# Kernel tuning notes

Measured on AMD Instinct MI355X. Metric: run time of the kernel, lower is better.

The kernel has to match this reference:

```python
import jax, jax.numpy as jnp
import numpy as np

N_NODES = 50000
N_EDGES = 800000
VOCAB = 1000
EMBED = 64
HIDDEN = 64
N_CLASSES = 10
N_GRAPHS = 512


def setup_inputs() -> dict:
    key = jax.random.key(0)
    ks = jax.random.split(key, 10)
    tokens = jax.random.randint(ks[0], (N_NODES,), 0, VOCAB)
    edge_index = jax.random.randint(ks[1], (2, N_EDGES), 0, N_NODES)
    batch = jnp.sort(jax.random.randint(ks[2], (N_NODES,), 0, N_GRAPHS))
    emb = jax.random.normal(ks[3], (VOCAB, EMBED), jnp.float32) * 0.02
    emb = emb.at[0].set(0.0)  # padding_idx=0
    W1 = jax.random.normal(ks[4], (EMBED, HIDDEN), jnp.float32) * (1.0 / np.sqrt(EMBED))
    b1 = jnp.zeros((HIDDEN,), jnp.float32)
    W2 = jax.random.normal(ks[5], (HIDDEN, HIDDEN), jnp.float32) * (1.0 / np.sqrt(HIDDEN))
    b2 = jnp.zeros((HIDDEN,), jnp.float32)
    lin_W = jax.random.normal(ks[6], (HIDDEN, N_CLASSES), jnp.float32) * (1.0 / np.sqrt(HIDDEN))
    lin_b = jnp.zeros((N_CLASSES,), jnp.float32)
    return {"tokens": tokens, "edge_index": edge_index, "batch": batch,
            "emb": emb, "W1": W1, "b1": b1, "W2": W2, "b2": b2,
            "lin_W": lin_W, "lin_b": lin_b}


def _gcn_conv(x, src, dst, W, b, n_nodes):
    # PyG GCNConv: add self-loops, symmetric normalization D^-1/2 (A+I) D^-1/2
    ones = jnp.ones((src.shape[0],), x.dtype)
    deg = jax.ops.segment_sum(ones, dst, num_segments=n_nodes) + 1.0  # self-loop
    dis = jnp.where(deg > 0, jax.lax.rsqrt(deg), 0.0)
    h = x @ W  # linear first (no bias)
    coef = dis[src] * dis[dst]                      # [E]
    msg = h[src] * coef[:, None]                    # gather + scale
    agg = jax.ops.segment_sum(msg, dst, num_segments=n_nodes)
    agg = agg + h * (dis * dis)[:, None]            # self-loop message
    return agg + b


def reference(tokens, edge_index, batch, emb, W1, b1, W2, b2, lin_W, lin_b):
    src, dst = edge_index[0], edge_index[1]
    x = emb[tokens]                                  # [N, EMBED]
    x = jax.nn.relu(_gcn_conv(x, src, dst, W1, b1, N_NODES))
    x = jax.nn.relu(_gcn_conv(x, src, dst, W2, b2, N_NODES))
    # global_mean_pool over batch ids
    sums = jax.ops.segment_sum(x, batch, num_segments=N_GRAPHS)
    cnts = jax.ops.segment_sum(jnp.ones((x.shape[0],), x.dtype), batch, num_segments=N_GRAPHS)
    pooled = sums / jnp.maximum(cnts, 1.0)[:, None]  # [G, HIDDEN]
    return pooled @ lin_W + lin_b
```

## Files before the change

### kernel.cpp

```cpp
#include <hip/hip_runtime.h>

#define NGRAPHS 512
#define D 64
#define NCLS 10
#define MAXDEG 64
#define MDSH 6

__global__ void k_deg(const int* __restrict__ dst, int* __restrict__ degi,
                      int* __restrict__ rank, int E) {
  int i = blockIdx.x * blockDim.x + threadIdx.x;
  if (i < E) rank[i] = atomicAdd(&degi[dst[i]], 1);
}

__global__ __launch_bounds__(256) void k_fused2(
    const int* __restrict__ src, const int* __restrict__ dst,
    const int* __restrict__ rank, const int* __restrict__ tokens,
    int2* __restrict__ ec2, int E,
    const int* __restrict__ degi, float* __restrict__ dis, int n,
    const float* __restrict__ emb, const float* __restrict__ W1,
    float4* __restrict__ ht4, float4* __restrict__ h2pad, int ntok,
    int fillBlocks, int disBlocks, int tokBlocks) {
  if (blockIdx.x < fillBlocks) {
    int e = blockIdx.x * 256 + threadIdx.x;
    if (e < E) {
      int s = src[e];
      int rk = rank[e];
      if (rk < MAXDEG)
        ec2[((size_t)dst[e] << MDSH) + rk] = make_int2(s, tokens[s]);
    }
    return;
  }
  if (blockIdx.x < fillBlocks + disBlocks) {
    int i = (blockIdx.x - fillBlocks) * 256 + threadIdx.x;
    if (i < n) dis[i] = rsqrtf((float)degi[i] + 1.0f);
    if (blockIdx.x == fillBlocks) {
      int t = threadIdx.x;
      if (t == 0) dis[n] = 0.0f;
      float4 z = make_float4(0.f, 0.f, 0.f, 0.f);
      if (t < 16) h2pad[((size_t)n << 4) + t] = z;
      else if (t < 32) ht4[((size_t)ntok << 4) + (t - 16)] = z;
    }
    return;
  }
  __shared__ float Ws[64 * 64];
  int tid = threadIdx.x;
  for (int i = tid; i < 64 * 64; i += 256) Ws[i] = W1[i];
  __syncthreads();
  const float4* Ws4 = (const float4*)Ws;
  int w = tid >> 6, lane = tid & 63;
  int cg = lane & 15;
  int kb = lane & 48;
  int bid = blockIdx.x - fillBlocks - disBlocks;
  for (int tok = bid * 4 + w; tok < ntok; tok += tokBlocks * 4) {
    float xval = emb[(size_t)tok * D + lane];
    float4 acc = make_float4(0.f, 0.f, 0.f, 0.f);
#pragma unroll
    for (int p = 0; p < 16; ++p) {
      float xv = __shfl(xval, kb + p, 64);
      float4 wv = Ws4[(kb + p) * 16 + cg];
      acc.x += xv * wv.x; acc.y += xv * wv.y;
      acc.z += xv * wv.z; acc.w += xv * wv.w;
    }
    acc.x += __shfl_xor(acc.x, 16, 64); acc.y += __shfl_xor(acc.y, 16, 64);
    acc.z += __shfl_xor(acc.z, 16, 64); acc.w += __shfl_xor(acc.w, 16, 64);
    acc.x += __shfl_xor(acc.x, 32, 64); acc.y += __shfl_xor(acc.y, 32, 64);
    acc.z += __shfl_xor(acc.z, 32, 64); acc.w += __shfl_xor(acc.w, 32, 64);
    if (lane < 16) ht4[(size_t)tok * 16 + cg] = acc;
  }
}

__global__ __launch_bounds__(256) void k_agg1g(const float4* __restrict__ ht4,
                                               const int2* __restrict__ ec2,
                                               const int* __restrict__ degi,
                                               const int* __restrict__ tokens,
                                               const float* __restrict__ dis,
                                               const float4* __restrict__ b14,
                                               const float* __restrict__ W2,
                                               float4* __restrict__ h2, int n,
                                               int ntok) {
  __shared__ float Ws[64 * 64];
  int tid = threadIdx.x;
  for (int i = tid; i < 64 * 64; i += 256) Ws[i] = W2[i];
  __syncthreads();
  const float4* Ws4 = (const float4*)Ws;
  int w = tid >> 6, lane = tid & 63;
  int slot = lane >> 4, cg = lane & 15;
  int kb = lane & 48;
  for (int node = blockIdx.x * 4 + w; node < n; node += gridDim.x * 4) {
    int deg = min(degi[node], MAXDEG);
    int beg = node << MDSH;
    int endp = beg + deg;
    float4 acc = make_float4(0.f, 0.f, 0.f, 0.f);
    int rounds = (deg + 31) >> 5;
    int j = beg + slot;
    for (int r = 0; r < rounds; ++r, j += 32) {
      int i0 = j, i1 = j + 4, i2 = j + 8, i3 = j + 12,
          i4 = j + 16, i5 = j + 20, i6 = j + 24, i7 = j + 28;
      int2 e0 = ec2[i0], e1 = ec2[i1], e2 = ec2[i2], e3 = ec2[i3];
      int2 e4 = ec2[i4], e5 = ec2[i5], e6 = ec2[i6], e7 = ec2[i7];
      int s0 = i0 < endp ? e0.x : n, t0 = i0 < endp ? e0.y : ntok;
      int s1 = i1 < endp ? e1.x : n, t1 = i1 < endp ? e1.y : ntok;
      int s2 = i2 < endp ? e2.x : n, t2 = i2 < endp ? e2.y : ntok;
      int s3 = i3 < endp ? e3.x : n, t3 = i3 < endp ? e3.y : ntok;
      int s4 = i4 < endp ? e4.x : n, t4 = i4 < endp ? e4.y : ntok;
      int s5 = i5 < endp ? e5.x : n, t5 = i5 < endp ? e5.y : ntok;
      int s6 = i6 < endp ? e6.x : n, t6 = i6 < endp ? e6.y : ntok;
      int s7 = i7 < endp ? e7.x : n, t7 = i7 < endp ? e7.y : ntok;
      float w0 = dis[s0], w1 = dis[s1], w2 = dis[s2], w3 = dis[s3];
      float w4 = dis[s4], w5 = dis[s5], w6 = dis[s6], w7 = dis[s7];
      float4 v0 = ht4[((size_t)t0 << 4) + cg];
      float4 v1 = ht4[((size_t)t1 << 4) + cg];
      float4 v2 = ht4[((size_t)t2 << 4) + cg];
      float4 v3 = ht4[((size_t)t3 << 4) + cg];
      float4 v4 = ht4[((size_t)t4 << 4) + cg];
      float4 v5 = ht4[((size_t)t5 << 4) + cg];
      float4 v6 = ht4[((size_t)t6 << 4) + cg];
      float4 v7 = ht4[((size_t)t7 << 4) + cg];
      acc.x += w0 * v0.x + w1 * v1.x + w2 * v2.x + w3 * v3.x
             + w4 * v4.x + w5 * v5.x + w6 * v6.x + w7 * v7.x;
      acc.y += w0 * v0.y + w1 * v1.y + w2 * v2.y + w3 * v3.y
             + w4 * v4.y + w5 * v5.y + w6 * v6.y + w7 * v7.y;
      acc.z += w0 * v0.z + w1 * v1.z + w2 * v2.z + w3 * v3.z
             + w4 * v4.z + w5 * v5.z + w6 * v6.z + w7 * v7.z;
      acc.w += w0 * v0.w + w1 * v1.w + w2 * v2.w + w3 * v3.w
             + w4 * v4.w + w5 * v5.w + w6 * v6.w + w7 * v7.w;
    }
    acc.x += __shfl_xor(acc.x, 16, 64); acc.y += __shfl_xor(acc.y, 16, 64);
    acc.z += __shfl_xor(acc.z, 16, 64); acc.w += __shfl_xor(acc.w, 16, 64);
    acc.x += __shfl_xor(acc.x, 32, 64); acc.y += __shfl_xor(acc.y, 32, 64);
    acc.z += __shfl_xor(acc.z, 32, 64); acc.w += __shfl_xor(acc.w, 32, 64);
    float dd = dis[node];
    float4 vd = ht4[((size_t)tokens[node] << 4) + cg];
    float4 bv = b14[cg];
    float4 x2;
    x2.x = dd * fmaxf(dd * (acc.x + dd * vd.x) + bv.x, 0.f);
    x2.y = dd * fmaxf(dd * (acc.y + dd * vd.y) + bv.y, 0.f);
    x2.z = dd * fmaxf(dd * (acc.z + dd * vd.z) + bv.z, 0.f);
    x2.w = dd * fmaxf(dd * (acc.w + dd * vd.w) + bv.w, 0.f);
    float4 g = make_float4(0.f, 0.f, 0.f, 0.f);
#pragma unroll
    for (int p = 0; p < 4; ++p) {
      int sl = (kb >> 2) + p;
      float xv0 = __shfl(x2.x, sl, 64);
      float xv1 = __shfl(x2.y, sl, 64);
      float xv2 = __shfl(x2.z, sl, 64);
      float xv3 = __shfl(x2.w, sl, 64);
      float4 w0 = Ws4[(kb + 4 * p + 0) * 16 + cg];
      float4 w1 = Ws4[(kb + 4 * p + 1) * 16 + cg];
      float4 w2 = Ws4[(kb + 4 * p + 2) * 16 + cg];
      float4 w3 = Ws4[(kb + 4 * p + 3) * 16 + cg];
      g.x += xv0 * w0.x + xv1 * w1.x + xv2 * w2.x + xv3 * w3.x;
      g.y += xv0 * w0.y + xv1 * w1.y + xv2 * w2.y + xv3 * w3.y;
      g.z += xv0 * w0.z + xv1 * w1.z + xv2 * w2.z + xv3 * w3.z;
      g.w += xv0 * w0.w + xv1 * w1.w + xv2 * w2.w + xv3 * w3.w;
    }
    g.x += __shfl_xor(g.x, 16, 64); g.y += __shfl_xor(g.y, 16, 64);
    g.z += __shfl_xor(g.z, 16, 64); g.w += __shfl_xor(g.w, 16, 64);
    g.x += __shfl_xor(g.x, 32, 64); g.y += __shfl_xor(g.y, 32, 64);
    g.z += __shfl_xor(g.z, 32, 64); g.w += __shfl_xor(g.w, 32, 64);
    if (lane < 16) h2[((size_t)node << 4) + cg] = g;
  }
}

__global__ __launch_bounds__(256) void k_aggs(const float4* __restrict__ h4,
                                              const int2* __restrict__ ec2,
                                              const int* __restrict__ degi,
                                              const float* __restrict__ dis,
                                              const float4* __restrict__ b24,
                                              float4* __restrict__ out, int n) {
  int tid = blockIdx.x * blockDim.x + threadIdx.x;
  int node = tid >> 6;
  int lane = tid & 63;
  int slot = lane >> 4;
  int cg = lane & 15;
  if (node >= n) return;
  int deg = min(degi[node], MAXDEG);
  int beg = node << MDSH;
  int endp = beg + deg;
  float4 acc = make_float4(0.f, 0.f, 0.f, 0.f);
  int rounds = (deg + 31) >> 5;
  int j = beg + slot;
  for (int r = 0; r < rounds; ++r, j += 32) {
    int i0 = j, i1 = j + 4, i2 = j + 8, i3 = j + 12,
        i4 = j + 16, i5 = j + 20, i6 = j + 24, i7 = j + 28;
    int2 e0 = ec2[i0], e1 = ec2[i1], e2 = ec2[i2], e3 = ec2[i3];
    int2 e4 = ec2[i4], e5 = ec2[i5], e6 = ec2[i6], e7 = ec2[i7];
    int s0 = i0 < endp ? e0.x : n;
    int s1 = i1 < endp ? e1.x : n;
    int s2 = i2 < endp ? e2.x : n;
    int s3 = i3 < endp ? e3.x : n;
    int s4 = i4 < endp ? e4.x : n;
    int s5 = i5 < endp ? e5.x : n;
    int s6 = i6 < endp ? e6.x : n;
    int s7 = i7 < endp ? e7.x : n;
    float4 v0 = h4[((size_t)s0 << 4) + cg];
    float4 v1 = h4[((size_t)s1 << 4) + cg];
    float4 v2 = h4[((size_t)s2 << 4) + cg];
    float4 v3 = h4[((size_t)s3 << 4) + cg];
    float4 v4 = h4[((size_t)s4 << 4) + cg];
    float4 v5 = h4[((size_t)s5 << 4) + cg];
    float4 v6 = h4[((size_t)s6 << 4) + cg];
    float4 v7 = h4[((size_t)s7 << 4) + cg];
    acc.x += ((v0.x + v1.x) + (v2.x + v3.x)) + ((v4.x + v5.x) + (v6.x + v7.x));
    acc.y += ((v0.y + v1.y) + (v2.y + v3.y)) + ((v4.y + v5.y) + (v6.y + v7.y));
    acc.z += ((v0.z + v1.z) + (v2.z + v3.z)) + ((v4.z + v5.z) + (v6.z + v7.z));
    acc.w += ((v0.w + v1.w) + (v2.w + v3.w)) + ((v4.w + v5.w) + (v6.w + v7.w));
  }
  acc.x += __shfl_xor(acc.x, 16, 64); acc.y += __shfl_xor(acc.y, 16, 64);
  acc.z += __shfl_xor(acc.z, 16, 64); acc.w += __shfl_xor(acc.w, 16, 64);
  acc.x += __shfl_xor(acc.x, 32, 64); acc.y += __shfl_xor(acc.y, 32, 64);
  acc.z += __shfl_xor(acc.z, 32, 64); acc.w += __shfl_xor(acc.w, 32, 64);
  if (slot == 0) {
    float dd = dis[node];
    float4 hv = h4[((size_t)node << 4) + cg];
    float4 bv = b24[cg];
    acc.x = fmaxf(dd * (acc.x + hv.x) + bv.x, 0.f);
    acc.y = fmaxf(dd * (acc.y + hv.y) + bv.y, 0.f);
    acc.z = fmaxf(dd * (acc.z + hv.z) + bv.z, 0.f);
    acc.w = fmaxf(dd * (acc.w + hv.w) + bv.w, 0.f);
    out[((size_t)node << 4) + cg] = acc;
  }
}

__device__ __forceinline__ int lower_bound(const int* __restrict__ a, int n, int v) {
  int lo = 0, hi = n;
  while (lo < hi) {
    int m = (lo + hi) >> 1;
    if (a[m] < v) lo = m + 1; else hi = m;
  }
  return lo;
}

__global__ __launch_bounds__(256) void k_poolfinal(const float* __restrict__ x,
                                                   const int* __restrict__ batch,
                                                   const float* __restrict__ lw,
                                                   const float* __restrict__ lb,
                                                   float* __restrict__ out, int n) {
  __shared__ float red[4][64];
  __shared__ float pooled[64];
  int g = blockIdx.x;
  int s = lower_bound(batch, n, g);
  int e = lower_bound(batch, n, g + 1);
  int w = threadIdx.x >> 6, lane = threadIdx.x & 63;
  float acc = 0.f;
  for (int i = s + w; i < e; i += 4) acc += x[(size_t)i * D + lane];
  red[w][lane] = acc;
  __syncthreads();
  if (w == 0) {
    float v = red[0][lane] + red[1][lane] + red[2][lane] + red[3][lane];
    pooled[lane] = v / fmaxf((float)(e - s), 1.0f);
  }
  __syncthreads();
  if (threadIdx.x < NCLS) {
    int c = threadIdx.x;
    float a = lb[c];
#pragma unroll
    for (int k = 0; k < D; ++k) a += pooled[k] * lw[k * NCLS + c];
    out[g * NCLS + c] = a;
  }
}

extern "C" void kernel_launch(void* const* d_in, const int* in_sizes, int n_in,
                              void* d_out, int out_size, void* d_ws, size_t ws_size,
                              hipStream_t stream) {
  const int* tokens = (const int*)d_in[0];
  const int* edge   = (const int*)d_in[1];
  const int* batch  = (const int*)d_in[2];
  const float* emb  = (const float*)d_in[3];
  const float* W1   = (const float*)d_in[4];
  const float* b1   = (const float*)d_in[5];
  const float* W2   = (const float*)d_in[6];
  const float* b2   = (const float*)d_in[7];
  const float* lw   = (const float*)d_in[8];
  const float* lb   = (const float*)d_in[9];
  float* out = (float*)d_out;

  const int N = in_sizes[0];
  const int E = in_sizes[1] / 2;
  const int ntok = in_sizes[3] / D;
  const int* src  = edge;
  const int* dstv = edge + E;

  char* ws = (char*)d_ws;
  size_t off = 0;
  auto alloc = [&](size_t bytes) {
    void* p = ws + off;
    off += (bytes + 255) & ~(size_t)255;
    return p;
  };
  float* A    = (float*)alloc((size_t)(N + 1) * D * sizeof(float));
  float* B    = (float*)alloc((size_t)N * D * sizeof(float));
  int2*  ec2  = (int2*)alloc((size_t)N * MAXDEG * sizeof(int2));
  int*   rank = (int*)alloc((size_t)E * sizeof(int));
  float* dis  = (float*)alloc((size_t)(N + 1) * sizeof(float));
  int*   degi = (int*)alloc((size_t)N * sizeof(int));
  float* ht   = (float*)alloc((size_t)(ntok + 1) * D * sizeof(float));

  hipMemsetAsync(degi, 0, (size_t)N * sizeof(int), stream);

  k_deg<<<(E + 255) / 256, 256, 0, stream>>>(dstv, degi, rank, E);

  const int fillBlocks = (E + 255) / 256;
  const int disBlocks = (N + 255) / 256;
  const int tokBlocks = (ntok + 3) / 4;
  k_fused2<<<fillBlocks + disBlocks + tokBlocks, 256, 0, stream>>>(
      src, dstv, rank, tokens, ec2, E, degi, dis, N, emb, W1, (float4*)ht,
      (float4*)A, ntok, fillBlocks, disBlocks, tokBlocks);

  k_agg1g<<<2048, 256, 0, stream>>>((const float4*)ht, ec2, degi, tokens, dis,
                                    (const float4*)b1, W2, (float4*)A, N, ntok);

  const int nodeBlocks = (N + 3) / 4;
  k_aggs<<<nodeBlocks, 256, 0, stream>>>((const float4*)A, ec2, degi, dis,
                                         (const float4*)b2, (float4*)B, N);

  k_poolfinal<<<NGRAPHS, 256, 0, stream>>>(B, batch, lw, lb, out, N);
}
```

Measured before the change: 157.6 us.

## Split layer-1 aggregation and W2 GEMM into separate kernels

The fused kernel that aggregated layer-1 messages and then applied W2 per node is split in two. One kernel does the one-node-per-wave aggregation with bias, ReLU and scaling and writes the result to a buffer. A second persistent kernel then multiplies that buffer by W2 held in shared memory. This lets the aggregation run as a flat, non-persistent grid without the shared-memory load, at the cost of an extra launch and an extra N×64 write and read round-trip through memory.

Result: slower. 161.3 us (+2.4%).

```diff
diff --git a/kernel.cpp b/kernel.cpp
--- a/kernel.cpp
+++ b/kernel.cpp
@@ -69,96 +69,101 @@
   }
 }
 
-__global__ __launch_bounds__(256) void k_agg1g(const float4* __restrict__ ht4,
+__global__ __launch_bounds__(256) void k_agg1t(const float4* __restrict__ ht4,
                                                const int2* __restrict__ ec2,
                                                const int* __restrict__ degi,
                                                const int* __restrict__ tokens,
                                                const float* __restrict__ dis,
                                                const float4* __restrict__ b14,
-                                               const float* __restrict__ W2,
-                                               float4* __restrict__ h2, int n,
+                                               float4* __restrict__ out, int n,
                                                int ntok) {
+  int tid = blockIdx.x * blockDim.x + threadIdx.x;
+  int node = tid >> 6;
+  int lane = tid & 63;
+  int slot = lane >> 4;
+  int cg = lane & 15;
+  if (node >= n) return;
+  int deg = min(degi[node], MAXDEG);
+  int beg = node << MDSH;
+  int endp = beg + deg;
+  float4 acc = make_float4(0.f, 0.f, 0.f, 0.f);
+  int rounds = (deg + 31) >> 5;
+  int j = beg + slot;
+  for (int r = 0; r < rounds; ++r, j += 32) {
+    int i0 = j, i1 = j + 4, i2 = j + 8, i3 = j + 12,
+        i4 = j + 16, i5 = j + 20, i6 = j + 24, i7 = j + 28;
+    int2 e0 = ec2[i0], e1 = ec2[i1], e2 = ec2[i2], e3 = ec2[i3];
+    int2 e4 = ec2[i4], e5 = ec2[i5], e6 = ec2[i6], e7 = ec2[i7];
+    int s0 = i0 < endp ? e0.x : n, t0 = i0 < endp ? e0.y : ntok;
+    int s1 = i1 < endp ? e1.x : n, t1 = i1 < endp ? e1.y : ntok;
+    int s2 = i2 < endp ? e2.x : n, t2 = i2 < endp ? e2.y : ntok;
+    int s3 = i3 < endp ? e3.x : n, t3 = i3 < endp ? e3.y : ntok;
+    int s4 = i4 < endp ? e4.x : n, t4 = i4 < endp ? e4.y : ntok;
+    int s5 = i5 < endp ? e5.x : n, t5 = i5 < endp ? e5.y : ntok;
+    int s6 = i6 < endp ? e6.x : n, t6 = i6 < endp ? e6.y : ntok;
+    int s7 = i7 < endp ? e7.x : n, t7 = i7 < endp ? e7.y : ntok;
+    float w0 = dis[s0], w1 = dis[s1], w2 = dis[s2], w3 = dis[s3];
+    float w4 = dis[s4], w5 = dis[s5], w6 = dis[s6], w7 = dis[s7];
+    float4 v0 = ht4[((size_t)t0 << 4) + cg];
+    float4 v1 = ht4[((size_t)t1 << 4) + cg];
+    float4 v2 = ht4[((size_t)t2 << 4) + cg];
+    float4 v3 = ht4[((size_t)t3 << 4) + cg];
+    float4 v4 = ht4[((size_t)t4 << 4) + cg];
+    float4 v5 = ht4[((size_t)t5 << 4) + cg];
+    float4 v6 = ht4[((size_t)t6 << 4) + cg];
+    float4 v7 = ht4[((size_t)t7 << 4) + cg];
+    acc.x += w0 * v0.x + w1 * v1.x + w2 * v2.x + w3 * v3.x
+           + w4 * v4.x + w5 * v5.x + w6 * v6.x + w7 * v7.x;
+    acc.y += w0 * v0.y + w1 * v1.y + w2 * v2.y + w3 * v3.y
+           + w4 * v4.y + w5 * v5.y + w6 * v6.y + w7 * v7.y;
+    acc.z += w0 * v0.z + w1 * v1.z + w2 * v2.z + w3 * v3.z
+           + w4 * v4.z + w5 * v5.z + w6 * v6.z + w7 * v7.z;
+    acc.w += w0 * v0.w + w1 * v1.w + w2 * v2.w + w3 * v3.w
+           + w4 * v4.w + w5 * v5.w + w6 * v6.w + w7 * v7.w;
+  }
+  acc.x += __shfl_xor(acc.x, 16, 64); acc.y += __shfl_xor(acc.y, 16, 64);
+  acc.z += __shfl_xor(acc.z, 16, 64); acc.w += __shfl_xor(acc.w, 16, 64);
+  acc.x += __shfl_xor(acc.x, 32, 64); acc.y += __shfl_xor(acc.y, 32, 64);
+  acc.z += __shfl_xor(acc.z, 32, 64); acc.w += __shfl_xor(acc.w, 32, 64);
+  if (slot == 0) {
+    float dd = dis[node];
+    float4 vd = ht4[((size_t)tokens[node] << 4) + cg];
+    float4 bv = b14[cg];
+    float4 r;
+    r.x = dd * fmaxf(dd * (acc.x + dd * vd.x) + bv.x, 0.f);
+    r.y = dd * fmaxf(dd * (acc.y + dd * vd.y) + bv.y, 0.f);
+    r.z = dd * fmaxf(dd * (acc.z + dd * vd.z) + bv.z, 0.f);
+    r.w = dd * fmaxf(dd * (acc.w + dd * vd.w) + bv.w, 0.f);
+    out[((size_t)node << 4) + cg] = r;
+  }
+}
+
+__global__ __launch_bounds__(256) void k_gemmp(const float* __restrict__ x,
+                                               const float* __restrict__ W,
+                                               float4* __restrict__ o4, int n) {
   __shared__ float Ws[64 * 64];
   int tid = threadIdx.x;
-  for (int i = tid; i < 64 * 64; i += 256) Ws[i] = W2[i];
+  for (int i = tid; i < 64 * 64; i += 256) Ws[i] = W[i];
   __syncthreads();
   const float4* Ws4 = (const float4*)Ws;
   int w = tid >> 6, lane = tid & 63;
-  int slot = lane >> 4, cg = lane & 15;
+  int cg = lane & 15;
   int kb = lane & 48;
   for (int node = blockIdx.x * 4 + w; node < n; node += gridDim.x * 4) {
-    int deg = min(degi[node], MAXDEG);
-    int beg = node << MDSH;
-    int endp = beg + deg;
+    float xval = x[(size_t)node * D + lane];
     float4 acc = make_float4(0.f, 0.f, 0.f, 0.f);
-    int rounds = (deg + 31) >> 5;
-    int j = beg + slot;
-    for (int r = 0; r < rounds; ++r, j += 32) {
-      int i0 = j, i1 = j + 4, i2 = j + 8, i3 = j + 12,
-          i4 = j + 16, i5 = j + 20, i6 = j + 24, i7 = j + 28;
-      int2 e0 = ec2[i0], e1 = ec2[i1], e2 = ec2[i2], e3 = ec2[i3];
-      int2 e4 = ec2[i4], e5 = ec2[i5], e6 = ec2[i6], e7 = ec2[i7];
-      int s0 = i0 < endp ? e0.x : n, t0 = i0 < endp ? e0.y : ntok;
-      int s1 = i1 < endp ? e1.x : n, t1 = i1 < endp ? e1.y : ntok;
-      int s2 = i2 < endp ? e2.x : n, t2 = i2 < endp ? e2.y : ntok;
-      int s3 = i3 < endp ? e3.x : n, t3 = i3 < endp ? e3.y : ntok;
-      int s4 = i4 < endp ? e4.x : n, t4 = i4 < endp ? e4.y : ntok;
-      int s5 = i5 < endp ? e5.x : n, t5 = i5 < endp ? e5.y : ntok;
-      int s6 = i6 < endp ? e6.x : n, t6 = i6 < endp ? e6.y : ntok;
-      int s7 = i7 < endp ? e7.x : n, t7 = i7 < endp ? e7.y : ntok;
-      float w0 = dis[s0], w1 = dis[s1], w2 = dis[s2], w3 = dis[s3];
-      float w4 = dis[s4], w5 = dis[s5], w6 = dis[s6], w7 = dis[s7];
-      float4 v0 = ht4[((size_t)t0 << 4) + cg];
-      float4 v1 = ht4[((size_t)t1 << 4) + cg];
-      float4 v2 = ht4[((size_t)t2 << 4) + cg];
-      float4 v3 = ht4[((size_t)t3 << 4) + cg];
-      float4 v4 = ht4[((size_t)t4 << 4) + cg];
-      float4 v5 = ht4[((size_t)t5 << 4) + cg];
-      float4 v6 = ht4[((size_t)t6 << 4) + cg];
-      float4 v7 = ht4[((size_t)t7 << 4) + cg];
-      acc.x += w0 * v0.x + w1 * v1.x + w2 * v2.x + w3 * v3.x
-             + w4 * v4.x + w5 * v5.x + w6 * v6.x + w7 * v7.x;
-      acc.y += w0 * v0.y + w1 * v1.y + w2 * v2.y + w3 * v3.y
-             + w4 * v4.y + w5 * v5.y + w6 * v6.y + w7 * v7.y;
-      acc.z += w0 * v0.z + w1 * v1.z + w2 * v2.z + w3 * v3.z
-             + w4 * v4.z + w5 * v5.z + w6 * v6.z + w7 * v7.z;
-      acc.w += w0 * v0.w + w1 * v1.w + w2 * v2.w + w3 * v3.w
-             + w4 * v4.w + w5 * v5.w + w6 * v6.w + w7 * v7.w;
+#pragma unroll
+    for (int p = 0; p < 16; ++p) {
+      float xv = __shfl(xval, kb + p, 64);
+      float4 wv = Ws4[(kb + p) * 16 + cg];
+      acc.x += xv * wv.x; acc.y += xv * wv.y;
+      acc.z += xv * wv.z; acc.w += xv * wv.w;
     }
     acc.x += __shfl_xor(acc.x, 16, 64); acc.y += __shfl_xor(acc.y, 16, 64);
     acc.z += __shfl_xor(acc.z, 16, 64); acc.w += __shfl_xor(acc.w, 16, 64);
     acc.x += __shfl_xor(acc.x, 32, 64); acc.y += __shfl_xor(acc.y, 32, 64);
     acc.z += __shfl_xor(acc.z, 32, 64); acc.w += __shfl_xor(acc.w, 32, 64);
-    float dd = dis[node];
-    float4 vd = ht4[((size_t)tokens[node] << 4) + cg];
-    float4 bv = b14[cg];
-    float4 x2;
-    x2.x = dd * fmaxf(dd * (acc.x + dd * vd.x) + bv.x, 0.f);
-    x2.y = dd * fmaxf(dd * (acc.y + dd * vd.y) + bv.y, 0.f);
-    x2.z = dd * fmaxf(dd * (acc.z + dd * vd.z) + bv.z, 0.f);
-    x2.w = dd * fmaxf(dd * (acc.w + dd * vd.w) + bv.w, 0.f);
-    float4 g = make_float4(0.f, 0.f, 0.f, 0.f);
-#pragma unroll
-    for (int p = 0; p < 4; ++p) {
-      int sl = (kb >> 2) + p;
-      float xv0 = __shfl(x2.x, sl, 64);
-      float xv1 = __shfl(x2.y, sl, 64);
-      float xv2 = __shfl(x2.z, sl, 64);
-      float xv3 = __shfl(x2.w, sl, 64);
-      float4 w0 = Ws4[(kb + 4 * p + 0) * 16 + cg];
-      float4 w1 = Ws4[(kb + 4 * p + 1) * 16 + cg];
-      float4 w2 = Ws4[(kb + 4 * p + 2) * 16 + cg];
-      float4 w3 = Ws4[(kb + 4 * p + 3) * 16 + cg];
-      g.x += xv0 * w0.x + xv1 * w1.x + xv2 * w2.x + xv3 * w3.x;
-      g.y += xv0 * w0.y + xv1 * w1.y + xv2 * w2.y + xv3 * w3.y;
-      g.z += xv0 * w0.z + xv1 * w1.z + xv2 * w2.z + xv3 * w3.z;
-      g.w += xv0 * w0.w + xv1 * w1.w + xv2 * w2.w + xv3 * w3.w;
-    }
-    g.x += __shfl_xor(g.x, 16, 64); g.y += __shfl_xor(g.y, 16, 64);
-    g.z += __shfl_xor(g.z, 16, 64); g.w += __shfl_xor(g.w, 16, 64);
-    g.x += __shfl_xor(g.x, 32, 64); g.y += __shfl_xor(g.y, 32, 64);
-    g.z += __shfl_xor(g.z, 32, 64); g.w += __shfl_xor(g.w, 32, 64);
-    if (lane < 16) h2[((size_t)node << 4) + cg] = g;
+    if (lane < 16) o4[(size_t)node * 16 + cg] = acc;
   }
 }
 
@@ -307,10 +312,13 @@
       src, dstv, rank, tokens, ec2, E, degi, dis, N, emb, W1, (float4*)ht,
       (float4*)A, ntok, fillBlocks, disBlocks, tokBlocks);
 
-  k_agg1g<<<2048, 256, 0, stream>>>((const float4*)ht, ec2, degi, tokens, dis,
-                                    (const float4*)b1, W2, (float4*)A, N, ntok);
-
   const int nodeBlocks = (N + 3) / 4;
+
+  k_agg1t<<<nodeBlocks, 256, 0, stream>>>((const float4*)ht, ec2, degi, tokens,
+                                          dis, (const float4*)b1, (float4*)B, N, ntok);
+
+  k_gemmp<<<2048, 256, 0, stream>>>(B, W2, (float4*)A, N);
+
   k_aggs<<<nodeBlocks, 256, 0, stream>>>((const float4*)A, ec2, degi, dis,
                                          (const float4*)b2, (float4*)B, N);
 
```
